# Performance work log

Measured on AMD Instinct MI355X. Metric: run time of the kernel, lower is better.

Reference implementation:

```python
import jax, jax.numpy as jnp
import numpy as np

LN_EPS = 1e-5
SA_EPS = 1e-8
NUM_ITERS = 3

def layer_norm(x, w, b):
    mu = jnp.mean(x, axis=-1, keepdims=True)
    var = jnp.mean((x - mu) ** 2, axis=-1, keepdims=True)
    return (x - mu) / jnp.sqrt(var + LN_EPS) * w + b


def setup_inputs() -> dict:
    key = jax.random.key(0)
    ks = jax.random.split(key, 24)
    B, C, H, W = 128, 256, 32, 32
    D, S, MH, NC = 64, 8, 128, 15
    s = lambda k, shape, scale=0.02: jax.random.normal(k, shape, dtype=jnp.float32) * scale
    inp = {
        "x1": jax.random.normal(ks[0], (B, C, H, W), dtype=jnp.float32),
        "x2": jax.random.normal(ks[1], (B, C, H, W), dtype=jnp.float32),
        # 1x1 convs stored as [out,in]
        "conv1_w": s(ks[2], (D, C)), "conv1_b": jnp.zeros((D,), jnp.float32),
        "conv2_w": s(ks[3], (D, C)), "conv2_b": jnp.zeros((D,), jnp.float32),
        "norm_w": jnp.ones((D,), jnp.float32), "norm_b": jnp.zeros((D,), jnp.float32),
        "ni_w": jnp.ones((D,), jnp.float32), "ni_b": jnp.zeros((D,), jnp.float32),
        "ns_w": jnp.ones((D,), jnp.float32), "ns_b": jnp.zeros((D,), jnp.float32),
        "nm_w": jnp.ones((D,), jnp.float32), "nm_b": jnp.zeros((D,), jnp.float32),
        "slots_mu": s(ks[4], (1, 1, D), 1.0), "slots_log_sigma": s(ks[5], (1, 1, D), 0.1),
        "Wq": s(ks[6], (D, D), 0.1), "Wk": s(ks[7], (D, D), 0.1), "Wv": s(ks[8], (D, D), 0.1),
        "gru_wih": s(ks[9], (3 * D, D), 0.1), "gru_whh": s(ks[10], (3 * D, D), 0.1),
        "gru_bih": jnp.zeros((3 * D,), jnp.float32), "gru_bhh": jnp.zeros((3 * D,), jnp.float32),
        "mlp_w1": s(ks[11], (MH, D), 0.1), "mlp_b1": jnp.zeros((MH,), jnp.float32),
        "mlp_w2": s(ks[12], (D, MH), 0.1), "mlp_b2": jnp.zeros((D,), jnp.float32),
        "head_w": s(ks[13], (NC, D), 0.1), "head_b": jnp.zeros((NC,), jnp.float32),
        "noise": jax.random.normal(ks[14], (B, S, D), dtype=jnp.float32),
    }
    return inp


def _forward(x1, x2, conv1_w, conv1_b, conv2_w, conv2_b, norm_w, norm_b,
             ni_w, ni_b, ns_w, ns_b, nm_w, nm_b, slots_mu, slots_log_sigma,
             Wq, Wk, Wv, gru_wih, gru_whh, gru_bih, gru_bhh,
             mlp_w1, mlp_b1, mlp_w2, mlp_b2, head_w, head_b, noise):
    B = x1.shape[0]
    D = Wq.shape[0]
    # 1x1 convs then flatten to tokens: [B, H*W, D]
    t1 = jnp.einsum('bchw,dc->bhwd', x1, conv1_w).reshape(B, -1, D) + conv1_b
    t2 = jnp.einsum('bchw,dc->bhwd', x2, conv2_w).reshape(B, -1, D) + conv2_b
    inputs = jnp.concatenate([t1, t2], axis=1)          # [B, N, D]
    inputs = layer_norm(inputs, norm_w, norm_b)

    # SlotAttention
    inputs = layer_norm(inputs, ni_w, ni_b)
    k = inputs @ Wk.T                                    # [B, N, D]
    v = inputs @ Wv.T
    slots = slots_mu + jnp.exp(slots_log_sigma) * noise  # [B, S, D]
    scale = D ** -0.5
    for _ in range(NUM_ITERS):
        slots_prev = slots
        sn = layer_norm(slots, ns_w, ns_b)
        q = (sn @ Wq.T) * scale                          # [B, S, D]
        attn_logits = jnp.einsum('bnd,bsd->bns', k, q)   # [B, N, S]
        attn = jax.nn.softmax(attn_logits, axis=-1) + SA_EPS
        attn = attn / jnp.sum(attn, axis=-2, keepdims=True)
        updates = jnp.einsum('bns,bnd->bsd', attn, v)    # [B, S, D]
        # GRUCell (torch gate order: r, z, n)
        gi = updates @ gru_wih.T + gru_bih               # [B, S, 3D]
        gh = slots_prev @ gru_whh.T + gru_bhh
        ir, iz, inn = jnp.split(gi, 3, axis=-1)
        hr, hz, hn = jnp.split(gh, 3, axis=-1)
        r = jax.nn.sigmoid(ir + hr)
        z = jax.nn.sigmoid(iz + hz)
        n = jnp.tanh(inn + r * hn)
        slots = (1.0 - z) * n + z * slots_prev
        # residual MLP
        h = layer_norm(slots, nm_w, nm_b)
        h = jax.nn.relu(h @ mlp_w1.T + mlp_b1) @ mlp_w2.T + mlp_b2
        slots = slots + h

    fused = jnp.mean(slots, axis=1)                      # [B, D]
    return fused @ head_w.T + head_b                     # [B, n_classes]


def reference(x1, x2, conv1_w, conv1_b, conv2_w, conv2_b, norm_w, norm_b,
              ni_w, ni_b, ns_w, ns_b, nm_w, nm_b, slots_mu, slots_log_sigma,
              Wq, Wk, Wv, gru_wih, gru_whh, gru_bih, gru_bhh,
              mlp_w1, mlp_b1, mlp_w2, mlp_b2, head_w, head_b, noise):
    return _forward(x1, x2, conv1_w, conv1_b, conv2_w, conv2_b, norm_w, norm_b,
                    ni_w, ni_b, ns_w, ns_b, nm_w, nm_b, slots_mu, slots_log_sigma,
                    Wq, Wk, Wv, gru_wih, gru_whh, gru_bih, gru_bhh,
                    mlp_w1, mlp_b1, mlp_w2, mlp_b2, head_w, head_b, noise)
```

## Files before the change

### kernel.cpp

```cpp
#include <hip/hip_runtime.h>
#include <stdint.h>


typedef __bf16 bf16;
typedef __bf16 bf16x8 __attribute__((ext_vector_type(8)));
typedef float  f32x4  __attribute__((ext_vector_type(4)));

#define MFMA16(a, b, c) __builtin_amdgcn_mfma_f32_16x16x32_bf16((a), (b), (c), 0, 0, 0)

#define ASYNC_LDS16(g, l) \
  __builtin_amdgcn_global_load_lds((const __attribute__((address_space(1))) void*)(g), \
                                   (__attribute__((address_space(3))) void*)(l), 16, 0, 0)

__global__ __launch_bounds__(256) void k0_convert(
    const float* __restrict__ c1w, const float* __restrict__ c2w,
    const float* __restrict__ wk,  const float* __restrict__ wvv,
    bf16* __restrict__ wconv, bf16* __restrict__ wkv)
{
  const int i = blockIdx.x * 256 + threadIdx.x;
  if (i < 16384) {
    wconv[i]         = (bf16)c1w[i];
    wconv[16384 + i] = (bf16)c2w[i];
  }
  if (i < 4096) {
    wkv[i]        = (bf16)wk[i];
    wkv[4096 + i] = (bf16)wvv[i];
  }
}

__global__ __launch_bounds__(256) void k1_conv_kv(
    const float* __restrict__ x1, const float* __restrict__ x2,
    const float* __restrict__ c1b, const float* __restrict__ c2b,
    const float* __restrict__ nw,  const float* __restrict__ nb,
    const float* __restrict__ niw, const float* __restrict__ nib,
    const bf16* __restrict__ wconv, const bf16* __restrict__ wkv,
    bf16* __restrict__ kbuf, bf16* __restrict__ vbuf)
{
  __shared__ union {
    float xs[64 * 264];
    struct { float T[64][65]; bf16 tok[64][72]; } p2;
  } U;

  const int bx   = blockIdx.x;
  const int tile = bx & 15;
  const int img  = (bx >> 4) & 1;
  const int b    = bx >> 5;
  const int tid  = threadIdx.x;
  const int lane = tid & 63;
  const int wvid = tid >> 6;
  const int l15  = lane & 15;
  const int quad = lane >> 4;

  {
    const float* xp = (img ? x2 : x1) + (size_t)b * (256 * 1024) + tile * 64;
    const int rowin = lane >> 4;
    const int pq    = (lane & 15) * 4;
    const float* ga0 = xp + (size_t)rowin * 1024 + pq;
    #pragma unroll
    for (int gi = 0; gi < 16; ++gi) {
      const int g = wvid + gi * 4;
      ASYNC_LDS16(ga0 + (size_t)g * 4096, &U.xs[g * 264]);
    }
  }
  __syncthreads();

  f32x4 acc[4] = {{0.f,0.f,0.f,0.f},{0.f,0.f,0.f,0.f},{0.f,0.f,0.f,0.f},{0.f,0.f,0.f,0.f}};
  {
    const bf16* wc = wconv + img * (64 * 256);
    const int p = wvid * 16 + l15;
    #pragma unroll
    for (int k0 = 0; k0 < 256; k0 += 32) {
      bf16x8 af;
      #pragma unroll
      for (int j = 0; j < 8; ++j) {
        const int c = k0 + quad * 8 + j;
        af[j] = (bf16)U.xs[(c >> 2) * 264 + (c & 3) * 64 + p];
      }
      #pragma unroll
      for (int nt = 0; nt < 4; ++nt) {
        const bf16x8 bw = *(const bf16x8*)&wc[(nt * 16 + l15) * 256 + k0 + quad * 8];
        acc[nt] = MFMA16(af, bw, acc[nt]);
      }
    }
  }
  __syncthreads();

  {
    const float* cb = img ? c2b : c1b;
    #pragma unroll
    for (int nt = 0; nt < 4; ++nt) {
      const int d = nt * 16 + l15;
      const float bias = cb[d];
      #pragma unroll
      for (int r = 0; r < 4; ++r)
        U.p2.T[wvid * 16 + quad * 4 + r][d] = acc[nt][r] + bias;
    }
  }
  __syncthreads();

  {
    const int pix = tid >> 2, part = tid & 3;
    float xv[16], yv[16];
    float s = 0.f, s2 = 0.f;
    #pragma unroll
    for (int i = 0; i < 16; ++i) {
      xv[i] = U.p2.T[pix][part * 16 + i];
      s += xv[i]; s2 += xv[i] * xv[i];
    }
    s  += __shfl_xor(s, 1);  s  += __shfl_xor(s, 2);
    s2 += __shfl_xor(s2, 1); s2 += __shfl_xor(s2, 2);
    float mu   = s * 0.015625f;
    float rstd = rsqrtf(s2 * 0.015625f - mu * mu + 1e-5f);
    s = 0.f; s2 = 0.f;
    #pragma unroll
    for (int i = 0; i < 16; ++i) {
      const int d = part * 16 + i;
      const float y = (xv[i] - mu) * rstd * nw[d] + nb[d];
      yv[i] = y; s += y; s2 += y * y;
    }
    s  += __shfl_xor(s, 1);  s  += __shfl_xor(s, 2);
    s2 += __shfl_xor(s2, 1); s2 += __shfl_xor(s2, 2);
    mu   = s * 0.015625f;
    rstd = rsqrtf(s2 * 0.015625f - mu * mu + 1e-5f);
    #pragma unroll
    for (int i = 0; i < 16; ++i) {
      const int d = part * 16 + i;
      U.p2.tok[pix][d] = (bf16)((yv[i] - mu) * rstd * niw[d] + nib[d]);
    }
  }
  __syncthreads();

  f32x4 ak[4] = {{0.f,0.f,0.f,0.f},{0.f,0.f,0.f,0.f},{0.f,0.f,0.f,0.f},{0.f,0.f,0.f,0.f}};
  f32x4 av[4] = {{0.f,0.f,0.f,0.f},{0.f,0.f,0.f,0.f},{0.f,0.f,0.f,0.f},{0.f,0.f,0.f,0.f}};
  #pragma unroll
  for (int k0 = 0; k0 < 64; k0 += 32) {
    const bf16x8 af = *(const bf16x8*)&U.p2.tok[wvid * 16 + l15][k0 + quad * 8];
    #pragma unroll
    for (int nt = 0; nt < 4; ++nt) {
      const bf16x8 bk = *(const bf16x8*)&wkv[(nt * 16 + l15) * 64 + k0 + quad * 8];
      const bf16x8 bv = *(const bf16x8*)&wkv[4096 + (nt * 16 + l15) * 64 + k0 + quad * 8];
      ak[nt] = MFMA16(af, bk, ak[nt]);
      av[nt] = MFMA16(af, bv, av[nt]);
    }
  }
  const size_t base = ((size_t)b * 2048 + img * 1024 + tile * 64) * 64;
  __syncthreads();
  #pragma unroll
  for (int nt = 0; nt < 4; ++nt)
    #pragma unroll
    for (int r = 0; r < 4; ++r)
      U.p2.T[wvid * 16 + quad * 4 + r][nt * 16 + l15] = ak[nt][r];
  __syncthreads();
  {
    const int pix = tid >> 2, dd = (tid & 3) * 16;
    bf16 tb[16];
    #pragma unroll
    for (int i = 0; i < 16; ++i) tb[i] = (bf16)U.p2.T[pix][dd + i];
    *(bf16x8*)&kbuf[base + (size_t)pix * 64 + dd]     = *(bf16x8*)&tb[0];
    *(bf16x8*)&kbuf[base + (size_t)pix * 64 + dd + 8] = *(bf16x8*)&tb[8];
  }
  __syncthreads();
  #pragma unroll
  for (int nt = 0; nt < 4; ++nt)
    #pragma unroll
    for (int r = 0; r < 4; ++r)
      U.p2.T[wvid * 16 + quad * 4 + r][nt * 16 + l15] = av[nt][r];
  __syncthreads();
  {
    const int pix = tid >> 2, dd = (tid & 3) * 16;
    bf16 tb[16];
    #pragma unroll
    for (int i = 0; i < 16; ++i) tb[i] = (bf16)U.p2.T[pix][dd + i];
    *(bf16x8*)&vbuf[base + (size_t)pix * 64 + dd]     = *(bf16x8*)&tb[0];
    *(bf16x8*)&vbuf[base + (size_t)pix * 64 + dd + 8] = *(bf16x8*)&tb[8];
  }
}

__global__ __launch_bounds__(512) void kS0(
    const float* __restrict__ smu, const float* __restrict__ slog,
    const float* __restrict__ noise,
    const float* __restrict__ nsw, const float* __restrict__ nsb,
    const float* __restrict__ Wq,
    float* __restrict__ slotbuf, bf16* __restrict__ qbuf)
{
  __shared__ float slots[8][64], tmp[8][64], mus[8], rstds[8];
  const int b = blockIdx.x, tid = threadIdx.x;
  const int s0 = tid >> 6, d0 = tid & 63;
  const float sv = smu[d0] + expf(slog[d0]) * noise[((size_t)b * 8 + s0) * 64 + d0];
  slots[s0][d0] = sv;
  slotbuf[((size_t)b * 8 + s0) * 64 + d0] = sv;
  __syncthreads();
  if (tid < 8) {
    float s = 0.f, s2 = 0.f;
    for (int d = 0; d < 64; ++d) { const float v = slots[tid][d]; s += v; s2 += v * v; }
    const float mu = s * 0.015625f;
    mus[tid] = mu;
    rstds[tid] = rsqrtf(s2 * 0.015625f - mu * mu + 1e-5f);
  }
  __syncthreads();
  tmp[s0][d0] = (slots[s0][d0] - mus[s0]) * rstds[s0] * nsw[d0] + nsb[d0];
  __syncthreads();
  float a = 0.f;
  for (int d = 0; d < 64; ++d) a += tmp[s0][d] * Wq[d0 * 64 + d];
  qbuf[((size_t)b * 8 + s0) * 64 + d0] = (bf16)(a * 0.125f);
}

__global__ __launch_bounds__(256) void kA(
    const bf16* __restrict__ kbuf, const bf16* __restrict__ vbuf,
    const bf16* __restrict__ qbuf,
    float* __restrict__ updpart, float* __restrict__ colpart)
{
  __shared__ bf16  qs[16][72];
  __shared__ bf16  vs[128][64];
  __shared__ float attn[8][132];
  __shared__ float cspart[4][8];

  const int bx  = blockIdx.x;
  const int b   = bx >> 4, ch = bx & 15;
  const int tid = threadIdx.x;
  const int lane = tid & 63;
  const int wvid = tid >> 6;
  const int l15  = lane & 15;
  const int quad = lane >> 4;
  const size_t tokbase = (size_t)b * 2048 + ch * 128;

  {
    const bf16* vg = vbuf + tokbase * 64;
    bf16* vsf = &vs[0][0];
    #pragma unroll
    for (int r = 0; r < 4; ++r) {
      const int idx = r * 256 + tid;
      *(bf16x8*)&vsf[idx * 8] = *(const bf16x8*)&vg[idx * 8];
    }
    if (tid < 64) {
      const int s = tid >> 3, o = (tid & 7) * 8;
      *(bf16x8*)&qs[s][o] = *(const bf16x8*)&qbuf[((size_t)b * 8 + s) * 64 + o];
    } else if (tid < 128) {
      const int s = 8 + ((tid - 64) >> 3), o = ((tid - 64) & 7) * 8;
      uint32_t* zp = (uint32_t*)&qs[s][o];
      zp[0] = 0u; zp[1] = 0u; zp[2] = 0u; zp[3] = 0u;
    }
  }
  __syncthreads();

  {
    float cs = 0.f;
    #pragma unroll
    for (int ms = 0; ms < 2; ++ms) {
      const int t0 = wvid * 32 + ms * 16;
      const bf16* kr = kbuf + (tokbase + t0 + l15) * 64 + quad * 8;
      f32x4 lg = {0.f, 0.f, 0.f, 0.f};
      lg = MFMA16(*(const bf16x8*)&kr[0],  *(const bf16x8*)&qs[l15][quad * 8],      lg);
      lg = MFMA16(*(const bf16x8*)&kr[32], *(const bf16x8*)&qs[l15][32 + quad * 8], lg);
      #pragma unroll
      for (int r = 0; r < 4; ++r) {
        const float l = lg[r];
        float m = l;
        m = fmaxf(m, __shfl_xor(m, 1));
        m = fmaxf(m, __shfl_xor(m, 2));
        m = fmaxf(m, __shfl_xor(m, 4));
        const float e = expf(l - m);
        float ss = e;
        ss += __shfl_xor(ss, 1);
        ss += __shfl_xor(ss, 2);
        ss += __shfl_xor(ss, 4);
        const float at = e / ss + 1e-8f;
        if (l15 < 8) { attn[l15][t0 + quad * 4 + r] = at; cs += at; }
      }
    }
    cs += __shfl_xor(cs, 16);
    cs += __shfl_xor(cs, 32);
    if (lane < 8) cspart[wvid][lane] = cs;
  }
  __syncthreads();

  {
    const int d0 = tid & 63;
    const int sA = tid >> 6;
    float u0 = 0.f, u1 = 0.f;
    #pragma unroll 4
    for (int n = 0; n < 128; ++n) {
      const float vv = (float)vs[n][d0];
      u0 += attn[sA][n] * vv;
      u1 += attn[sA + 4][n] * vv;
    }
    float* up = updpart + ((size_t)b * 16 + ch) * 512;
    up[sA * 64 + d0]       = u0;
    up[(sA + 4) * 64 + d0] = u1;
    if (tid < 8)
      colpart[((size_t)b * 16 + ch) * 8 + tid] =
        cspart[0][tid] + cspart[1][tid] + cspart[2][tid] + cspart[3][tid];
  }
}

__global__ __launch_bounds__(512) void kB(
    const float* __restrict__ updpart, const float* __restrict__ colpart,
    float* __restrict__ slotbuf, bf16* __restrict__ qbuf,
    const float* __restrict__ nsw, const float* __restrict__ nsb,
    const float* __restrict__ nmw, const float* __restrict__ nmb,
    const float* __restrict__ Wq,
    const float* __restrict__ wih, const float* __restrict__ whh,
    const float* __restrict__ bih, const float* __restrict__ bhh,
    const float* __restrict__ w1,  const float* __restrict__ b1,
    const float* __restrict__ w2,  const float* __restrict__ b2,
    const float* __restrict__ hwt, const float* __restrict__ hb,
    float* __restrict__ out, const int last)
{
  __shared__ float slots[8][64], tmp[8][64];
  __shared__ union { float h1[8][128]; struct { float gi[8][192]; float gh[8][192]; } g; } ub;
  __shared__ float mus[8], rstds[8];
  const int b = blockIdx.x, tid = threadIdx.x;
  const int s0 = tid >> 6, d0 = tid & 63;

  {
    const float* up = updpart + (size_t)b * 16 * 512;
    float u = 0.f;
    #pragma unroll
    for (int ch = 0; ch < 16; ++ch) u += up[ch * 512 + s0 * 64 + d0];
    const float* cp = colpart + (size_t)b * 128;
    float cs = 0.f;
    #pragma unroll
    for (int ch = 0; ch < 16; ++ch) cs += cp[ch * 8 + s0];
    tmp[s0][d0] = u / cs;
    slots[s0][d0] = slotbuf[((size_t)b * 8 + s0) * 64 + d0];
  }
  __syncthreads();

  for (int idx = tid; idx < 1536; idx += 512) {
    const int s = idx / 192, j = idx % 192;
    float a = bih[j], h = bhh[j];
    for (int d = 0; d < 64; ++d) {
      a += tmp[s][d]   * wih[j * 64 + d];
      h += slots[s][d] * whh[j * 64 + d];
    }
    ub.g.gi[s][j] = a;
    ub.g.gh[s][j] = h;
  }
  __syncthreads();
  {
    const float r  = 1.f / (1.f + expf(-(ub.g.gi[s0][d0]       + ub.g.gh[s0][d0])));
    const float z  = 1.f / (1.f + expf(-(ub.g.gi[s0][64 + d0]  + ub.g.gh[s0][64 + d0])));
    const float nn = tanhf(ub.g.gi[s0][128 + d0] + r * ub.g.gh[s0][128 + d0]);
    slots[s0][d0] = (1.f - z) * nn + z * slots[s0][d0];
  }
  __syncthreads();

  if (tid < 8) {
    float s = 0.f, s2 = 0.f;
    for (int d = 0; d < 64; ++d) { const float v = slots[tid][d]; s += v; s2 += v * v; }
    const float mu = s * 0.015625f;
    mus[tid] = mu;
    rstds[tid] = rsqrtf(s2 * 0.015625f - mu * mu + 1e-5f);
  }
  __syncthreads();
  tmp[s0][d0] = (slots[s0][d0] - mus[s0]) * rstds[s0] * nmw[d0] + nmb[d0];
  __syncthreads();
  for (int idx = tid; idx < 1024; idx += 512) {
    const int s = idx >> 7, j = idx & 127;
    float a = b1[j];
    for (int d = 0; d < 64; ++d) a += tmp[s][d] * w1[j * 64 + d];
    ub.h1[s][j] = fmaxf(a, 0.f);
  }
  __syncthreads();
  {
    float a = b2[d0];
    for (int j = 0; j < 128; ++j) a += ub.h1[s0][j] * w2[d0 * 128 + j];
    slots[s0][d0] += a;
  }
  __syncthreads();

  slotbuf[((size_t)b * 8 + s0) * 64 + d0] = slots[s0][d0];

  if (!last) {
    if (tid < 8) {
      float s = 0.f, s2 = 0.f;
      for (int d = 0; d < 64; ++d) { const float v = slots[tid][d]; s += v; s2 += v * v; }
      const float mu = s * 0.015625f;
      mus[tid] = mu;
      rstds[tid] = rsqrtf(s2 * 0.015625f - mu * mu + 1e-5f);
    }
    __syncthreads();
    tmp[s0][d0] = (slots[s0][d0] - mus[s0]) * rstds[s0] * nsw[d0] + nsb[d0];
    __syncthreads();
    float a = 0.f;
    for (int d = 0; d < 64; ++d) a += tmp[s0][d] * Wq[d0 * 64 + d];
    qbuf[((size_t)b * 8 + s0) * 64 + d0] = (bf16)(a * 0.125f);
  } else {
    if (tid < 64) {
      float f = 0.f;
      #pragma unroll
      for (int s = 0; s < 8; ++s) f += slots[s][tid];
      ((float*)tmp)[tid] = f * 0.125f;
    }
    __syncthreads();
    if (tid < 15) {
      float a = hb[tid];
      for (int d = 0; d < 64; ++d) a += ((float*)tmp)[d] * hwt[tid * 64 + d];
      out[b * 15 + tid] = a;
    }
  }
}

extern "C" void kernel_launch(void* const* d_in, const int* in_sizes, int n_in,
                              void* d_out, int out_size, void* d_ws, size_t ws_size,
                              hipStream_t stream) {
  const float* x1   = (const float*)d_in[0];
  const float* x2   = (const float*)d_in[1];
  const float* c1w  = (const float*)d_in[2];
  const float* c1b  = (const float*)d_in[3];
  const float* c2w  = (const float*)d_in[4];
  const float* c2b  = (const float*)d_in[5];
  const float* nw   = (const float*)d_in[6];
  const float* nb   = (const float*)d_in[7];
  const float* niw  = (const float*)d_in[8];
  const float* nib  = (const float*)d_in[9];
  const float* nsw  = (const float*)d_in[10];
  const float* nsb  = (const float*)d_in[11];
  const float* nmw  = (const float*)d_in[12];
  const float* nmb  = (const float*)d_in[13];
  const float* smu  = (const float*)d_in[14];
  const float* slog = (const float*)d_in[15];
  const float* Wq   = (const float*)d_in[16];
  const float* Wk   = (const float*)d_in[17];
  const float* Wv   = (const float*)d_in[18];
  const float* wih  = (const float*)d_in[19];
  const float* whh  = (const float*)d_in[20];
  const float* bih  = (const float*)d_in[21];
  const float* bhh  = (const float*)d_in[22];
  const float* w1   = (const float*)d_in[23];
  const float* b1   = (const float*)d_in[24];
  const float* w2   = (const float*)d_in[25];
  const float* b2   = (const float*)d_in[26];
  const float* hwt  = (const float*)d_in[27];
  const float* hb   = (const float*)d_in[28];
  const float* noise= (const float*)d_in[29];

  char* ws = (char*)d_ws;
  bf16*  kbuf    = (bf16*)(ws);
  bf16*  vbuf    = (bf16*)(ws + (size_t)33554432);
  bf16*  wconv   = (bf16*)(ws + (size_t)67108864);
  bf16*  wkv     = (bf16*)(ws + (size_t)67174400);
  float* slotbuf = (float*)(ws + (size_t)67190784);
  bf16*  qbuf    = (bf16*)(ws + (size_t)67452928);
  float* updpart = (float*)(ws + (size_t)67584000);
  float* colpart = (float*)(ws + (size_t)71778304);

  k0_convert<<<dim3(64), dim3(256), 0, stream>>>(c1w, c2w, Wk, Wv, wconv, wkv);
  k1_conv_kv<<<dim3(4096), dim3(256), 0, stream>>>(x1, x2, c1b, c2b, nw, nb, niw, nib,
                                                   wconv, wkv, kbuf, vbuf);
  kS0<<<dim3(128), dim3(512), 0, stream>>>(smu, slog, noise, nsw, nsb, Wq, slotbuf, qbuf);
  for (int it = 0; it < 3; ++it) {
    kA<<<dim3(2048), dim3(256), 0, stream>>>(kbuf, vbuf, qbuf, updpart, colpart);
    kB<<<dim3(128), dim3(512), 0, stream>>>(updpart, colpart, slotbuf, qbuf,
                                            nsw, nsb, nmw, nmb, Wq,
                                            wih, whh, bih, bhh, w1, b1, w2, b2,
                                            hwt, hb, (float*)d_out, (it == 2) ? 1 : 0);
  }
}
```

Baseline: 609.0 us.

## Transpose V layout, use MFMA for attention update, restructure slot kernels

The conv-kv kernel now stages input in two halves, which halves the LDS footprint so more blocks can be resident, and it writes V transposed as [B,64,2048]. The attention kernel then computes attn@V with bf16 MFMA straight from global memory instead of a scalar FP32 loop over LDS. The slot kernels (kS0, kB) replace serial per-thread dot products and single-thread LayerNorm statistics with vectorized, shuffle-reduced dot products and warp-shuffle reductions. In exchange, attention weights are rounded to bf16 before the update and column sums, which slightly reduces precision.

```diff
diff --git a/kernel.cpp b/kernel.cpp
--- a/kernel.cpp
+++ b/kernel.cpp
@@ -34,11 +34,12 @@
     const float* __restrict__ nw,  const float* __restrict__ nb,
     const float* __restrict__ niw, const float* __restrict__ nib,
     const bf16* __restrict__ wconv, const bf16* __restrict__ wkv,
-    bf16* __restrict__ kbuf, bf16* __restrict__ vbuf)
+    bf16* __restrict__ kbuf, bf16* __restrict__ vT)
 {
   __shared__ union {
-    float xs[64 * 264];
+    float xs[32 * 264];
     struct { float T[64][65]; bf16 tok[64][72]; } p2;
+    struct { float Tk[64][65]; float Tv[64][65]; } kv;
   } U;
 
   const int bx   = blockIdx.x;
@@ -51,25 +52,24 @@
   const int l15  = lane & 15;
   const int quad = lane >> 4;
 
-  {
-    const float* xp = (img ? x2 : x1) + (size_t)b * (256 * 1024) + tile * 64;
-    const int rowin = lane >> 4;
-    const int pq    = (lane & 15) * 4;
-    const float* ga0 = xp + (size_t)rowin * 1024 + pq;
-    #pragma unroll
-    for (int gi = 0; gi < 16; ++gi) {
+  const float* xp  = (img ? x2 : x1) + (size_t)b * (256 * 1024) + tile * 64;
+  const int   rowin = lane >> 4;
+  const int   pq    = (lane & 15) * 4;
+  const float* ga0  = xp + (size_t)rowin * 1024 + pq;
+  const bf16* wc = wconv + img * (64 * 256);
+  const int p = wvid * 16 + l15;
+
+  f32x4 acc[4] = {{0.f,0.f,0.f,0.f},{0.f,0.f,0.f,0.f},{0.f,0.f,0.f,0.f},{0.f,0.f,0.f,0.f}};
+
+  for (int half = 0; half < 2; ++half) {
+    #pragma unroll
+    for (int gi = 0; gi < 8; ++gi) {
       const int g = wvid + gi * 4;
-      ASYNC_LDS16(ga0 + (size_t)g * 4096, &U.xs[g * 264]);
-    }
-  }
-  __syncthreads();
-
-  f32x4 acc[4] = {{0.f,0.f,0.f,0.f},{0.f,0.f,0.f,0.f},{0.f,0.f,0.f,0.f},{0.f,0.f,0.f,0.f}};
-  {
-    const bf16* wc = wconv + img * (64 * 256);
-    const int p = wvid * 16 + l15;
-    #pragma unroll
-    for (int k0 = 0; k0 < 256; k0 += 32) {
+      ASYNC_LDS16(ga0 + (size_t)(half * 128 + g * 4) * 1024, &U.xs[g * 264]);
+    }
+    __syncthreads();
+    #pragma unroll
+    for (int k0 = 0; k0 < 128; k0 += 32) {
       bf16x8 af;
       #pragma unroll
       for (int j = 0; j < 8; ++j) {
@@ -78,12 +78,12 @@
       }
       #pragma unroll
       for (int nt = 0; nt < 4; ++nt) {
-        const bf16x8 bw = *(const bf16x8*)&wc[(nt * 16 + l15) * 256 + k0 + quad * 8];
+        const bf16x8 bw = *(const bf16x8*)&wc[(nt * 16 + l15) * 256 + half * 128 + k0 + quad * 8];
         acc[nt] = MFMA16(af, bw, acc[nt]);
       }
     }
-  }
-  __syncthreads();
+    __syncthreads();
+  }
 
   {
     const float* cb = img ? c2b : c1b;
@@ -143,36 +143,29 @@
       av[nt] = MFMA16(af, bv, av[nt]);
     }
   }
-  const size_t base = ((size_t)b * 2048 + img * 1024 + tile * 64) * 64;
-  __syncthreads();
+  __syncthreads();
+
   #pragma unroll
   for (int nt = 0; nt < 4; ++nt)
     #pragma unroll
-    for (int r = 0; r < 4; ++r)
-      U.p2.T[wvid * 16 + quad * 4 + r][nt * 16 + l15] = ak[nt][r];
-  __syncthreads();
-  {
-    const int pix = tid >> 2, dd = (tid & 3) * 16;
+    for (int r = 0; r < 4; ++r) {
+      U.kv.Tk[wvid * 16 + quad * 4 + r][nt * 16 + l15] = ak[nt][r];
+      U.kv.Tv[nt * 16 + l15][wvid * 16 + quad * 4 + r] = av[nt][r];
+    }
+  __syncthreads();
+  {
+    const int row = tid >> 2, dd = (tid & 3) * 16;
+    const size_t kb = ((size_t)b * 2048 + img * 1024 + tile * 64) * 64;
     bf16 tb[16];
     #pragma unroll
-    for (int i = 0; i < 16; ++i) tb[i] = (bf16)U.p2.T[pix][dd + i];
-    *(bf16x8*)&kbuf[base + (size_t)pix * 64 + dd]     = *(bf16x8*)&tb[0];
-    *(bf16x8*)&kbuf[base + (size_t)pix * 64 + dd + 8] = *(bf16x8*)&tb[8];
-  }
-  __syncthreads();
-  #pragma unroll
-  for (int nt = 0; nt < 4; ++nt)
-    #pragma unroll
-    for (int r = 0; r < 4; ++r)
-      U.p2.T[wvid * 16 + quad * 4 + r][nt * 16 + l15] = av[nt][r];
-  __syncthreads();
-  {
-    const int pix = tid >> 2, dd = (tid & 3) * 16;
-    bf16 tb[16];
-    #pragma unroll
-    for (int i = 0; i < 16; ++i) tb[i] = (bf16)U.p2.T[pix][dd + i];
-    *(bf16x8*)&vbuf[base + (size_t)pix * 64 + dd]     = *(bf16x8*)&tb[0];
-    *(bf16x8*)&vbuf[base + (size_t)pix * 64 + dd + 8] = *(bf16x8*)&tb[8];
+    for (int i = 0; i < 16; ++i) tb[i] = (bf16)U.kv.Tk[row][dd + i];
+    *(bf16x8*)&kbuf[kb + (size_t)row * 64 + dd]     = *(bf16x8*)&tb[0];
+    *(bf16x8*)&kbuf[kb + (size_t)row * 64 + dd + 8] = *(bf16x8*)&tb[8];
+    #pragma unroll
+    for (int i = 0; i < 16; ++i) tb[i] = (bf16)U.kv.Tv[row][dd + i];
+    const size_t vb = ((size_t)b * 64 + row) * 2048 + img * 1024 + tile * 64 + dd;
+    *(bf16x8*)&vT[vb]     = *(bf16x8*)&tb[0];
+    *(bf16x8*)&vT[vb + 8] = *(bf16x8*)&tb[8];
   }
 }
 
@@ -183,71 +176,71 @@
     const float* __restrict__ Wq,
     float* __restrict__ slotbuf, bf16* __restrict__ qbuf)
 {
-  __shared__ float slots[8][64], tmp[8][64], mus[8], rstds[8];
+  __shared__ float tmp[8][66];
   const int b = blockIdx.x, tid = threadIdx.x;
   const int s0 = tid >> 6, d0 = tid & 63;
-  const float sv = smu[d0] + expf(slog[d0]) * noise[((size_t)b * 8 + s0) * 64 + d0];
-  slots[s0][d0] = sv;
-  slotbuf[((size_t)b * 8 + s0) * 64 + d0] = sv;
-  __syncthreads();
-  if (tid < 8) {
-    float s = 0.f, s2 = 0.f;
-    for (int d = 0; d < 64; ++d) { const float v = slots[tid][d]; s += v; s2 += v * v; }
-    const float mu = s * 0.015625f;
-    mus[tid] = mu;
-    rstds[tid] = rsqrtf(s2 * 0.015625f - mu * mu + 1e-5f);
-  }
-  __syncthreads();
-  tmp[s0][d0] = (slots[s0][d0] - mus[s0]) * rstds[s0] * nsw[d0] + nsb[d0];
-  __syncthreads();
-  float a = 0.f;
-  for (int d = 0; d < 64; ++d) a += tmp[s0][d] * Wq[d0 * 64 + d];
-  qbuf[((size_t)b * 8 + s0) * 64 + d0] = (bf16)(a * 0.125f);
+  const int part = tid & 7, sl = (tid >> 3) & 7, wv = tid >> 6;
+
+  const float sval = smu[d0] + expf(slog[d0]) * noise[((size_t)b * 8 + s0) * 64 + d0];
+  slotbuf[((size_t)b * 8 + s0) * 64 + d0] = sval;
+  float s = sval, s2 = sval * sval;
+  #pragma unroll
+  for (int m = 1; m < 64; m <<= 1) { s += __shfl_xor(s, m); s2 += __shfl_xor(s2, m); }
+  const float mu = s * 0.015625f;
+  const float rstd = rsqrtf(s2 * 0.015625f - mu * mu + 1e-5f);
+  tmp[s0][d0] = (sval - mu) * rstd * nsw[d0] + nsb[d0];
+  __syncthreads();
+
+  float tm[8];
+  #pragma unroll
+  for (int i = 0; i < 8; ++i) tm[i] = tmp[sl][part * 8 + i];
+  for (int orr = 0; orr < 8; ++orr) {
+    const int d = orr * 8 + wv;
+    const f32x4 w0 = *(const f32x4*)&Wq[d * 64 + part * 8];
+    const f32x4 w1v = *(const f32x4*)&Wq[d * 64 + part * 8 + 4];
+    float a = tm[0]*w0[0] + tm[1]*w0[1] + tm[2]*w0[2] + tm[3]*w0[3]
+            + tm[4]*w1v[0] + tm[5]*w1v[1] + tm[6]*w1v[2] + tm[7]*w1v[3];
+    a += __shfl_xor(a, 1); a += __shfl_xor(a, 2); a += __shfl_xor(a, 4);
+    if (part == 0) qbuf[((size_t)b * 8 + sl) * 64 + d] = (bf16)(a * 0.125f);
+  }
 }
 
 __global__ __launch_bounds__(256) void kA(
-    const bf16* __restrict__ kbuf, const bf16* __restrict__ vbuf,
+    const bf16* __restrict__ kbuf, const bf16* __restrict__ vT,
     const bf16* __restrict__ qbuf,
     float* __restrict__ updpart, float* __restrict__ colpart)
 {
   __shared__ bf16  qs[16][72];
-  __shared__ bf16  vs[128][64];
-  __shared__ float attn[8][132];
+  __shared__ bf16  attn_b[16][136];
+  __shared__ float updp[4][8][64];
   __shared__ float cspart[4][8];
 
   const int bx  = blockIdx.x;
   const int b   = bx >> 4, ch = bx & 15;
   const int tid = threadIdx.x;
-  const int lane = tid & 63;
-  const int wvid = tid >> 6;
-  const int l15  = lane & 15;
-  const int quad = lane >> 4;
+  const int lane = tid & 63, wvid = tid >> 6;
+  const int l15 = lane & 15, quad = lane >> 4;
   const size_t tokbase = (size_t)b * 2048 + ch * 128;
 
-  {
-    const bf16* vg = vbuf + tokbase * 64;
-    bf16* vsf = &vs[0][0];
-    #pragma unroll
-    for (int r = 0; r < 4; ++r) {
-      const int idx = r * 256 + tid;
-      *(bf16x8*)&vsf[idx * 8] = *(const bf16x8*)&vg[idx * 8];
-    }
-    if (tid < 64) {
-      const int s = tid >> 3, o = (tid & 7) * 8;
-      *(bf16x8*)&qs[s][o] = *(const bf16x8*)&qbuf[((size_t)b * 8 + s) * 64 + o];
-    } else if (tid < 128) {
-      const int s = 8 + ((tid - 64) >> 3), o = ((tid - 64) & 7) * 8;
-      uint32_t* zp = (uint32_t*)&qs[s][o];
-      zp[0] = 0u; zp[1] = 0u; zp[2] = 0u; zp[3] = 0u;
-    }
+  if (tid < 64) {
+    const int s = tid >> 3, o = (tid & 7) * 8;
+    *(bf16x8*)&qs[s][o] = *(const bf16x8*)&qbuf[((size_t)b * 8 + s) * 64 + o];
+  } else if (tid < 128) {
+    const int s = 8 + ((tid - 64) >> 3), o = ((tid - 64) & 7) * 8;
+    uint32_t* zp = (uint32_t*)&qs[s][o];
+    zp[0] = 0u; zp[1] = 0u; zp[2] = 0u; zp[3] = 0u;
+  }
+  {
+    uint32_t* az = (uint32_t*)&attn_b[8][0];
+    for (int i = tid; i < 544; i += 256) az[i] = 0u;
   }
   __syncthreads();
 
   {
     float cs = 0.f;
     #pragma unroll
-    for (int ms = 0; ms < 2; ++ms) {
-      const int t0 = wvid * 32 + ms * 16;
+    for (int mt = 0; mt < 2; ++mt) {
+      const int t0 = wvid * 32 + mt * 16;
       const bf16* kr = kbuf + (tokbase + t0 + l15) * 64 + quad * 8;
       f32x4 lg = {0.f, 0.f, 0.f, 0.f};
       lg = MFMA16(*(const bf16x8*)&kr[0],  *(const bf16x8*)&qs[l15][quad * 8],      lg);
@@ -265,7 +258,11 @@
         ss += __shfl_xor(ss, 2);
         ss += __shfl_xor(ss, 4);
         const float at = e / ss + 1e-8f;
-        if (l15 < 8) { attn[l15][t0 + quad * 4 + r] = at; cs += at; }
+        if (l15 < 8) {
+          const bf16 ab = (bf16)at;
+          attn_b[l15][t0 + quad * 4 + r] = ab;
+          cs += (float)ab;
+        }
       }
     }
     cs += __shfl_xor(cs, 16);
@@ -275,18 +272,27 @@
   __syncthreads();
 
   {
-    const int d0 = tid & 63;
-    const int sA = tid >> 6;
-    float u0 = 0.f, u1 = 0.f;
-    #pragma unroll 4
-    for (int n = 0; n < 128; ++n) {
-      const float vv = (float)vs[n][d0];
-      u0 += attn[sA][n] * vv;
-      u1 += attn[sA + 4][n] * vv;
-    }
-    float* up = updpart + ((size_t)b * 16 + ch) * 512;
-    up[sA * 64 + d0]       = u0;
-    up[(sA + 4) * 64 + d0] = u1;
+    const bf16x8 afr = *(const bf16x8*)&attn_b[l15][wvid * 32 + quad * 8];
+    const bf16* vrow = vT + (size_t)b * 131072 + (size_t)ch * 128 + wvid * 32 + quad * 8;
+    const f32x4 zero4 = {0.f, 0.f, 0.f, 0.f};
+    #pragma unroll
+    for (int nt = 0; nt < 4; ++nt) {
+      const bf16x8 bv = *(const bf16x8*)&vrow[(size_t)(nt * 16 + l15) * 2048];
+      f32x4 dd = MFMA16(afr, bv, zero4);
+      if (quad < 2) {
+        #pragma unroll
+        for (int r = 0; r < 4; ++r)
+          updp[wvid][quad * 4 + r][nt * 16 + l15] = dd[r];
+      }
+    }
+  }
+  __syncthreads();
+
+  {
+    const float* up = &updp[0][0][0];
+    float* og = updpart + ((size_t)b * 16 + ch) * 512;
+    for (int o = tid; o < 512; o += 256)
+      og[o] = up[o] + up[o + 512] + up[o + 1024] + up[o + 1536];
     if (tid < 8)
       colpart[((size_t)b * 16 + ch) * 8 + tid] =
         cspart[0][tid] + cspart[1][tid] + cspart[2][tid] + cspart[3][tid];
@@ -306,96 +312,131 @@
     const float* __restrict__ hwt, const float* __restrict__ hb,
     float* __restrict__ out, const int last)
 {
-  __shared__ float slots[8][64], tmp[8][64];
-  __shared__ union { float h1[8][128]; struct { float gi[8][192]; float gh[8][192]; } g; } ub;
-  __shared__ float mus[8], rstds[8];
+  __shared__ float slots[8][66];
+  __shared__ float tmp[8][66];
+  __shared__ float gig[8][192], ghg[8][192];
+  __shared__ float h1[8][132];
   const int b = blockIdx.x, tid = threadIdx.x;
   const int s0 = tid >> 6, d0 = tid & 63;
-
-  {
-    const float* up = updpart + (size_t)b * 16 * 512;
+  const int part = tid & 7, sl = (tid >> 3) & 7, wv = tid >> 6;
+
+  {
+    const float* up = updpart + (size_t)b * 8192 + s0 * 64 + d0;
     float u = 0.f;
     #pragma unroll
-    for (int ch = 0; ch < 16; ++ch) u += up[ch * 512 + s0 * 64 + d0];
-    const float* cp = colpart + (size_t)b * 128;
+    for (int ch = 0; ch < 16; ++ch) u += up[ch * 512];
+    const float* cp = colpart + (size_t)b * 128 + s0;
     float cs = 0.f;
     #pragma unroll
-    for (int ch = 0; ch < 16; ++ch) cs += cp[ch * 8 + s0];
+    for (int ch = 0; ch < 16; ++ch) cs += cp[ch * 8];
     tmp[s0][d0] = u / cs;
     slots[s0][d0] = slotbuf[((size_t)b * 8 + s0) * 64 + d0];
   }
   __syncthreads();
 
-  for (int idx = tid; idx < 1536; idx += 512) {
-    const int s = idx / 192, j = idx % 192;
-    float a = bih[j], h = bhh[j];
-    for (int d = 0; d < 64; ++d) {
-      a += tmp[s][d]   * wih[j * 64 + d];
-      h += slots[s][d] * whh[j * 64 + d];
-    }
-    ub.g.gi[s][j] = a;
-    ub.g.gh[s][j] = h;
-  }
-  __syncthreads();
-  {
-    const float r  = 1.f / (1.f + expf(-(ub.g.gi[s0][d0]       + ub.g.gh[s0][d0])));
-    const float z  = 1.f / (1.f + expf(-(ub.g.gi[s0][64 + d0]  + ub.g.gh[s0][64 + d0])));
-    const float nn = tanhf(ub.g.gi[s0][128 + d0] + r * ub.g.gh[s0][128 + d0]);
-    slots[s0][d0] = (1.f - z) * nn + z * slots[s0][d0];
-  }
-  __syncthreads();
-
-  if (tid < 8) {
-    float s = 0.f, s2 = 0.f;
-    for (int d = 0; d < 64; ++d) { const float v = slots[tid][d]; s += v; s2 += v * v; }
+  {
+    float tv[8], sv[8];
+    #pragma unroll
+    for (int i = 0; i < 8; ++i) { tv[i] = tmp[sl][part * 8 + i]; sv[i] = slots[sl][part * 8 + i]; }
+    for (int jr = 0; jr < 24; ++jr) {
+      const int j = jr * 8 + wv;
+      const f32x4 wa0 = *(const f32x4*)&wih[j * 64 + part * 8];
+      const f32x4 wa1 = *(const f32x4*)&wih[j * 64 + part * 8 + 4];
+      const f32x4 wb0 = *(const f32x4*)&whh[j * 64 + part * 8];
+      const f32x4 wb1 = *(const f32x4*)&whh[j * 64 + part * 8 + 4];
+      float a = tv[0]*wa0[0] + tv[1]*wa0[1] + tv[2]*wa0[2] + tv[3]*wa0[3]
+              + tv[4]*wa1[0] + tv[5]*wa1[1] + tv[6]*wa1[2] + tv[7]*wa1[3];
+      float h = sv[0]*wb0[0] + sv[1]*wb0[1] + sv[2]*wb0[2] + sv[3]*wb0[3]
+              + sv[4]*wb1[0] + sv[5]*wb1[1] + sv[6]*wb1[2] + sv[7]*wb1[3];
+      a += __shfl_xor(a, 1); a += __shfl_xor(a, 2); a += __shfl_xor(a, 4);
+      h += __shfl_xor(h, 1); h += __shfl_xor(h, 2); h += __shfl_xor(h, 4);
+      if (part == 0) { gig[sl][j] = a + bih[j]; ghg[sl][j] = h + bhh[j]; }
+    }
+  }
+  __syncthreads();
+
+  float snew;
+  {
+    const float r  = 1.f / (1.f + expf(-(gig[s0][d0]       + ghg[s0][d0])));
+    const float z  = 1.f / (1.f + expf(-(gig[s0][64 + d0]  + ghg[s0][64 + d0])));
+    const float nn = tanhf(gig[s0][128 + d0] + r * ghg[s0][128 + d0]);
+    snew = (1.f - z) * nn + z * slots[s0][d0];
+    slots[s0][d0] = snew;
+  }
+  {
+    float s = snew, s2 = snew * snew;
+    #pragma unroll
+    for (int m = 1; m < 64; m <<= 1) { s += __shfl_xor(s, m); s2 += __shfl_xor(s2, m); }
     const float mu = s * 0.015625f;
-    mus[tid] = mu;
-    rstds[tid] = rsqrtf(s2 * 0.015625f - mu * mu + 1e-5f);
-  }
-  __syncthreads();
-  tmp[s0][d0] = (slots[s0][d0] - mus[s0]) * rstds[s0] * nmw[d0] + nmb[d0];
-  __syncthreads();
-  for (int idx = tid; idx < 1024; idx += 512) {
-    const int s = idx >> 7, j = idx & 127;
-    float a = b1[j];
-    for (int d = 0; d < 64; ++d) a += tmp[s][d] * w1[j * 64 + d];
-    ub.h1[s][j] = fmaxf(a, 0.f);
-  }
-  __syncthreads();
-  {
-    float a = b2[d0];
-    for (int j = 0; j < 128; ++j) a += ub.h1[s0][j] * w2[d0 * 128 + j];
-    slots[s0][d0] += a;
-  }
-  __syncthreads();
-
-  slotbuf[((size_t)b * 8 + s0) * 64 + d0] = slots[s0][d0];
+    const float rstd = rsqrtf(s2 * 0.015625f - mu * mu + 1e-5f);
+    tmp[s0][d0] = (snew - mu) * rstd * nmw[d0] + nmb[d0];
+  }
+  __syncthreads();
+
+  {
+    float tm[8];
+    #pragma unroll
+    for (int i = 0; i < 8; ++i) tm[i] = tmp[sl][part * 8 + i];
+    for (int jr = 0; jr < 16; ++jr) {
+      const int j = jr * 8 + wv;
+      const f32x4 w0 = *(const f32x4*)&w1[j * 64 + part * 8];
+      const f32x4 w1v = *(const f32x4*)&w1[j * 64 + part * 8 + 4];
+      float a = tm[0]*w0[0] + tm[1]*w0[1] + tm[2]*w0[2] + tm[3]*w0[3]
+              + tm[4]*w1v[0] + tm[5]*w1v[1] + tm[6]*w1v[2] + tm[7]*w1v[3];
+      a += __shfl_xor(a, 1); a += __shfl_xor(a, 2); a += __shfl_xor(a, 4);
+      if (part == 0) h1[sl][j] = fmaxf(a + b1[j], 0.f);
+    }
+  }
+  __syncthreads();
+
+  for (int orr = 0; orr < 8; ++orr) {
+    const int d = orr * 8 + wv;
+    float a = 0.f;
+    #pragma unroll
+    for (int i = 0; i < 4; ++i) {
+      const f32x4 wv4 = *(const f32x4*)&w2[d * 128 + part * 16 + i * 4];
+      a += h1[sl][part * 16 + i * 4 + 0] * wv4[0] + h1[sl][part * 16 + i * 4 + 1] * wv4[1]
+         + h1[sl][part * 16 + i * 4 + 2] * wv4[2] + h1[sl][part * 16 + i * 4 + 3] * wv4[3];
+    }
+    a += __shfl_xor(a, 1); a += __shfl_xor(a, 2); a += __shfl_xor(a, 4);
+    if (part == 0) slots[sl][d] += a + b2[d];
+  }
+  __syncthreads();
+
+  const float sfin = slots[s0][d0];
+  slotbuf[((size_t)b * 8 + s0) * 64 + d0] = sfin;
 
   if (!last) {
-    if (tid < 8) {
-      float s = 0.f, s2 = 0.f;
-      for (int d = 0; d < 64; ++d) { const float v = slots[tid][d]; s += v; s2 += v * v; }
-      const float mu = s * 0.015625f;
-      mus[tid] = mu;
-      rstds[tid] = rsqrtf(s2 * 0.015625f - mu * mu + 1e-5f);
-    }
+    float s = sfin, s2 = sfin * sfin;
+    #pragma unroll
+    for (int m = 1; m < 64; m <<= 1) { s += __shfl_xor(s, m); s2 += __shfl_xor(s2, m); }
+    const float mu = s * 0.015625f;
+    const float rstd = rsqrtf(s2 * 0.015625f - mu * mu + 1e-5f);
+    tmp[s0][d0] = (sfin - mu) * rstd * nsw[d0] + nsb[d0];
     __syncthreads();
-    tmp[s0][d0] = (slots[s0][d0] - mus[s0]) * rstds[s0] * nsw[d0] + nsb[d0];
-    __syncthreads();
-    float a = 0.f;
-    for (int d = 0; d < 64; ++d) a += tmp[s0][d] * Wq[d0 * 64 + d];
-    qbuf[((size_t)b * 8 + s0) * 64 + d0] = (bf16)(a * 0.125f);
+    float tm[8];
+    #pragma unroll
+    for (int i = 0; i < 8; ++i) tm[i] = tmp[sl][part * 8 + i];
+    for (int orr = 0; orr < 8; ++orr) {
+      const int d = orr * 8 + wv;
+      const f32x4 w0 = *(const f32x4*)&Wq[d * 64 + part * 8];
+      const f32x4 w1v = *(const f32x4*)&Wq[d * 64 + part * 8 + 4];
+      float a = tm[0]*w0[0] + tm[1]*w0[1] + tm[2]*w0[2] + tm[3]*w0[3]
+              + tm[4]*w1v[0] + tm[5]*w1v[1] + tm[6]*w1v[2] + tm[7]*w1v[3];
+      a += __shfl_xor(a, 1); a += __shfl_xor(a, 2); a += __shfl_xor(a, 4);
+      if (part == 0) qbuf[((size_t)b * 8 + sl) * 64 + d] = (bf16)(a * 0.125f);
+    }
   } else {
     if (tid < 64) {
       float f = 0.f;
       #pragma unroll
       for (int s = 0; s < 8; ++s) f += slots[s][tid];
-      ((float*)tmp)[tid] = f * 0.125f;
+      tmp[0][tid] = f * 0.125f;
     }
     __syncthreads();
     if (tid < 15) {
       float a = hb[tid];
-      for (int d = 0; d < 64; ++d) a += ((float*)tmp)[d] * hwt[tid * 64 + d];
+      for (int d = 0; d < 64; ++d) a += tmp[0][d] * hwt[tid * 64 + d];
       out[b * 15 + tid] = a;
     }
   }
@@ -437,7 +478,7 @@
 
   char* ws = (char*)d_ws;
   bf16*  kbuf    = (bf16*)(ws);
-  bf16*  vbuf    = (bf16*)(ws + (size_t)33554432);
+  bf16*  vT      = (bf16*)(ws + (size_t)33554432);
   bf16*  wconv   = (bf16*)(ws + (size_t)67108864);
   bf16*  wkv     = (bf16*)(ws + (size_t)67174400);
   float* slotbuf = (float*)(ws + (size_t)67190784);
@@ -447,10 +488,10 @@
 
   k0_convert<<<dim3(64), dim3(256), 0, stream>>>(c1w, c2w, Wk, Wv, wconv, wkv);
   k1_conv_kv<<<dim3(4096), dim3(256), 0, stream>>>(x1, x2, c1b, c2b, nw, nb, niw, nib,
-                                                   wconv, wkv, kbuf, vbuf);
+                                                   wconv, wkv, kbuf, vT);
   kS0<<<dim3(128), dim3(512), 0, stream>>>(smu, slog, noise, nsw, nsb, Wq, slotbuf, qbuf);
   for (int it = 0; it < 3; ++it) {
-    kA<<<dim3(2048), dim3(256), 0, stream>>>(kbuf, vbuf, qbuf, updpart, colpart);
+    kA<<<dim3(2048), dim3(256), 0, stream>>>(kbuf, vT, qbuf, updpart, colpart);
     kB<<<dim3(128), dim3(512), 0, stream>>>(updpart, colpart, slotbuf, qbuf,
                                             nsw, nsb, nmw, nmb, Wq,
                                             wih, whh, bih, bhh, w1, b1, w2, b2,
```

Measured after the change: 523.9 us. 1.16x faster.
